# Optimization experiments

Hardware: AMD Instinct MI355X
Metric: run time of the kernel (lower is better)

## Reference

```python
import jax, jax.numpy as jnp
import numpy as np

HEAD = 16
H_DIM = 64  # dims // head
ROT = 32    # h_dim // 2


def setup_inputs() -> dict:
    key = jax.random.key(0)
    k1, k2, k3, k4 = jax.random.split(key, 4)
    B, S, D = 8, 4096, 1024
    x = jax.random.normal(k1, (B, S, D), dtype=jnp.float32)
    thetas = jax.random.normal(k2, (ROT,), dtype=jnp.float32) * 0.1
    theta_scale = jnp.ones((1,), dtype=jnp.float32)
    # near-orthogonal matrix, as r_matrix is initialized to eye
    r_matrix = jnp.eye(H_DIM, dtype=jnp.float32) + 0.01 * jax.random.normal(k3, (H_DIM, H_DIM), dtype=jnp.float32)
    base = 10000.0
    inv_freq = (1.0 / base ** (jnp.arange(0, H_DIM, 2, dtype=jnp.float32) / H_DIM)).astype(jnp.float32)
    # rotation plane index pairs (i, j) with i != j, as produced by update_pairs()
    i_idx = jax.random.randint(k4, (ROT,), 0, H_DIM)
    off = jax.random.randint(jax.random.fold_in(k4, 1), (ROT,), 1, H_DIM)
    j_idx = (i_idx + off) % H_DIM
    pairs = jnp.stack([i_idx, j_idx], axis=1).astype(jnp.int32)
    return {"x": x, "thetas": thetas, "theta_scale": theta_scale,
            "r_matrix": r_matrix, "inv_freq": inv_freq, "pairs": pairs}


def _blended_rotation(xf, pairs, thetas_scaled):
    """Apply rot sequential blended Givens rotations to xf [N, H_DIM].

    B = (G + H + R)/3 with G == R the Givens rotation in plane (i,j) and
    H = I - 2 v v^T (v = [cos, sin] in plane (i,j), ||v|| = 1).
    x @ B only changes columns i and j; all other columns pass through
    since (2*x_k + x_k)/3 = x_k. This is mathematically identical to the
    original dense h_dim x h_dim matmul per step.
    """
    def step(xc, inp):
        i, j, th = inp["i"], inp["j"], inp["th"]
        c, s = jnp.cos(th), jnp.sin(th)
        xi = jnp.take(xc, i, axis=1)
        xj = jnp.take(xc, j, axis=1)
        gi = xi * c + xj * s        # (x @ G) column i; also equals x . v
        gj = -xi * s + xj * c       # (x @ G) column j
        ni = (2.0 * gi + xi - 2.0 * gi * c) / 3.0
        nj = (2.0 * gj + xj - 2.0 * gi * s) / 3.0
        xc = xc.at[:, i].set(ni)
        xc = xc.at[:, j].set(nj)
        return xc, None
    xf, _ = jax.lax.scan(step, xf, {"i": pairs[:, 0], "j": pairs[:, 1], "th": thetas_scaled})
    return xf


def reference(x, thetas, theta_scale, r_matrix, inv_freq, pairs):
    B, S, D = x.shape
    xf = x.reshape(-1, H_DIM)                       # [B*S*head, h_dim]
    # adjusted_rot = int(round(rot_scale * rot)) == rot for rot_scale = 1
    xf = _blended_rotation(xf, pairs, thetas * theta_scale[0])
    xf = xf @ r_matrix
    xr = xf.reshape(B, S, HEAD, H_DIM)
    # RoPE-style sin/cos mix (note: concatenated halves, not interleaved)
    pos = jnp.arange(S, dtype=x.dtype)
    sinu = pos[:, None] * inv_freq[None, :]          # [S, h_dim/2]
    sin = jnp.sin(sinu)[None, :, None, :]
    cos = jnp.cos(sinu)[None, :, None, :]
    x1, x2 = xr[..., ::2], xr[..., 1::2]
    out = jnp.concatenate([x1 * cos - x2 * sin, x1 * sin + x2 * cos], axis=-1)
    return out.reshape(B, S, D)
```

## Files before the change

kernel.cpp:

```cpp
#include <hip/hip_runtime.h>

#define HEADS 16
#define HD 64
#define ROT 32
#define SEQ 4096
#define BROWS 256
#define PADW 33

typedef float sv16 __attribute__((ext_vector_type(16)));

__global__ __launch_bounds__(256) void build_W_kernel(
    const float* __restrict__ thetas,
    const float* __restrict__ theta_scale,
    const float* __restrict__ r_matrix,
    const int* __restrict__ pairs,
    float* __restrict__ Wp)
{
    __shared__ float M[64][65];
    __shared__ float Rl[64][65];
    const int tid = threadIdx.x;

    #pragma unroll
    for (int it = 0; it < 16; ++it) {
        const int f = it * 256 + tid;
        Rl[f >> 6][f & 63] = r_matrix[f];
    }

    if (tid < 64) {
        const int t = tid;
        #pragma unroll
        for (int k = 0; k < 64; ++k) M[t][k] = (k == t) ? 1.0f : 0.0f;
        const float scale = theta_scale[0];
        #pragma unroll 1
        for (int r = 0; r < ROT; ++r) {
            const int i = pairs[2 * r + 0];
            const int j = pairs[2 * r + 1];
            const float th = thetas[r] * scale;
            float s, c;
            sincosf(th, &s, &c);
            const float xi = M[t][i];
            const float xj = M[t][j];
            const float gi =  xi * c + xj * s;
            const float gj = -xi * s + xj * c;
            const float ni = (2.0f * gi + xi - 2.0f * gi * c) / 3.0f;
            const float nj = (2.0f * gj + xj - 2.0f * gi * s) / 3.0f;
            M[t][i] = ni;
            M[t][j] = nj;
        }
    }
    __syncthreads();

    const int n = tid & 63;
    const int kq = tid >> 6;
    const int cn = (n < 32) ? (2 * n) : (2 * (n - 32) + 1);
    #pragma unroll 1
    for (int kk = 0; kk < 16; ++kk) {
        const int k = kq * 16 + kk;
        float acc = 0.0f;
        #pragma unroll
        for (int j = 0; j < 64; ++j) acc = fmaf(M[k][j], Rl[j][cn], acc);
        Wp[k * 64 + n] = acc;
    }
}

__global__ __launch_bounds__(256, 4) void fused_main(
    const float* __restrict__ x,
    const float* __restrict__ Wp,
    const float* __restrict__ inv_freq,
    float* __restrict__ out)
{
    __shared__ float xs[BROWS * PADW];
    __shared__ float tc[16 * 33];
    __shared__ float tsn[16 * 33];

    const int tid = threadIdx.x;
    const int blk = blockIdx.x;
    const long long base4 = (long long)blk * (BROWS * HD / 4);
    const float4* __restrict__ xv = (const float4*)x + base4;
    float4* __restrict__ ov = (float4*)out + base4;

    {
        const int s0 = (blk & (SEQ / 16 - 1)) * 16;
        #pragma unroll
        for (int u = 0; u < 2; ++u) {
            const int e = tid * 2 + u;
            const int sl = e >> 5;
            const int f = e & 31;
            const float ang = (float)(s0 + sl) * inv_freq[f];
            float sn, cs;
            sincosf(ang, &sn, &cs);
            tc[sl * 33 + f] = cs;
            tsn[sl * 33 + f] = sn;
        }
    }

    float acc[64];
    #pragma unroll
    for (int nn = 0; nn < 64; ++nn) acc[nn] = 0.0f;

    #pragma unroll 1
    for (int half = 0; half < 2; ++half) {
        __syncthreads();
        #pragma unroll
        for (int it = 0; it < 8; ++it) {
            const int f = it * 256 + tid;
            const int row = f >> 3;
            const int c4 = f & 7;
            const float4 v = xv[row * 16 + half * 8 + c4];
            float* p = &xs[row * PADW + c4 * 4];
            p[0] = v.x; p[1] = v.y; p[2] = v.z; p[3] = v.w;
        }
        __syncthreads();

        const float* xrow = &xs[tid * PADW];
        #pragma unroll 1
        for (int kc = 0; kc < 2; ++kc) {
            float xk[16];
            #pragma unroll
            for (int m = 0; m < 16; ++m) xk[m] = xrow[kc * 16 + m];
            const int kbase = half * 32 + kc * 16;
            #pragma unroll
            for (int m = 0; m < 16; ++m) {
                const float* pm = Wp + (kbase + m) * 64;
                sv16 w0, w1, w2, w3;
                asm volatile(
                    "s_load_dwordx16 %0, %4, 0x0\n\t"
                    "s_load_dwordx16 %1, %4, 0x40\n\t"
                    "s_load_dwordx16 %2, %4, 0x80\n\t"
                    "s_load_dwordx16 %3, %4, 0xC0\n\t"
                    "s_waitcnt lgkmcnt(0)"
                    : "=&s"(w0), "=&s"(w1), "=&s"(w2), "=&s"(w3)
                    : "s"(pm));
                const float xm = xk[m];
                #pragma unroll
                for (int i = 0; i < 16; ++i) {
                    acc[i]      = fmaf(xm, w0[i], acc[i]);
                    acc[16 + i] = fmaf(xm, w1[i], acc[16 + i]);
                    acc[32 + i] = fmaf(xm, w2[i], acc[32 + i]);
                    acc[48 + i] = fmaf(xm, w3[i], acc[48 + i]);
                }
            }
        }
    }

    {
        const int sl = tid >> 4;
        #pragma unroll
        for (int n = 0; n < 32; ++n) {
            const float c = tc[sl * 33 + n];
            const float s = tsn[sl * 33 + n];
            const float a = acc[n];
            const float b = acc[32 + n];
            acc[n]      = a * c - b * s;
            acc[32 + n] = a * s + b * c;
        }
    }

    #pragma unroll 1
    for (int half = 0; half < 2; ++half) {
        __syncthreads();
        float* prow = &xs[tid * PADW];
        #pragma unroll
        for (int n = 0; n < 32; ++n) prow[n] = acc[half * 32 + n];
        __syncthreads();
        #pragma unroll
        for (int it = 0; it < 8; ++it) {
            const int f = it * 256 + tid;
            const int row = f >> 3;
            const int c4 = f & 7;
            const float* p = &xs[row * PADW + c4 * 4];
            ov[row * 16 + half * 8 + c4] = make_float4(p[0], p[1], p[2], p[3]);
        }
    }
}

extern "C" void kernel_launch(void* const* d_in, const int* in_sizes, int n_in,
                              void* d_out, int out_size, void* d_ws, size_t ws_size,
                              hipStream_t stream) {
    const float* x   = (const float*)d_in[0];
    const float* th  = (const float*)d_in[1];
    const float* sc  = (const float*)d_in[2];
    const float* R   = (const float*)d_in[3];
    const float* ivf = (const float*)d_in[4];
    const int*   pr  = (const int*)d_in[5];
    float* W = (float*)d_ws;

    build_W_kernel<<<1, 256, 0, stream>>>(th, sc, R, pr, W);

    const int rows = out_size / HD;
    const int blocks = rows / BROWS;
    fused_main<<<blocks, 256, 0, stream>>>(x, W, ivf, (float*)d_out);
}
```

Measured before the change: 342.6 us.

## Double-buffer scalar W loads and drop LDS staging for direct row I/O

The main kernel now double-buffers the scalar W row loads, so the next pair of rows is fetched while FMAs run on the current pair. Previously every row waited on all four loads before computing. It also removes the shared-memory staging of x and out: each thread reads and writes its own 64-float row directly as float4, and occupancy is raised to 5 blocks per CU. The W-builder kernel precomputes sincos and pair indices into shared memory in parallel. The risk is uncoalesced per-thread strided global access (256-byte row stride across lanes) and higher register pressure.

```diff
diff --git a/kernel.cpp b/kernel.cpp
--- a/kernel.cpp
+++ b/kernel.cpp
@@ -5,7 +5,6 @@
 #define ROT 32
 #define SEQ 4096
 #define BROWS 256
-#define PADW 33
 
 typedef float sv16 __attribute__((ext_vector_type(16)));
 
@@ -18,26 +17,36 @@
 {
     __shared__ float M[64][65];
     __shared__ float Rl[64][65];
+    __shared__ int   ip[32], jp[32];
+    __shared__ float cs[32], sn[32];
     const int tid = threadIdx.x;
 
+    if (tid < 32) {
+        const int i = pairs[2 * tid + 0];
+        const int j = pairs[2 * tid + 1];
+        float s, c;
+        sincosf(thetas[tid] * theta_scale[0], &s, &c);
+        ip[tid] = i; jp[tid] = j; cs[tid] = c; sn[tid] = s;
+    }
     #pragma unroll
     for (int it = 0; it < 16; ++it) {
         const int f = it * 256 + tid;
         Rl[f >> 6][f & 63] = r_matrix[f];
     }
+    if (tid < 64) {
+        #pragma unroll
+        for (int k = 0; k < 64; ++k) M[tid][k] = (k == tid) ? 1.0f : 0.0f;
+    }
+    __syncthreads();
 
     if (tid < 64) {
         const int t = tid;
-        #pragma unroll
-        for (int k = 0; k < 64; ++k) M[t][k] = (k == t) ? 1.0f : 0.0f;
-        const float scale = theta_scale[0];
         #pragma unroll 1
         for (int r = 0; r < ROT; ++r) {
-            const int i = pairs[2 * r + 0];
-            const int j = pairs[2 * r + 1];
-            const float th = thetas[r] * scale;
-            float s, c;
-            sincosf(th, &s, &c);
+            const int i = ip[r];
+            const int j = jp[r];
+            const float c = cs[r];
+            const float s = sn[r];
             const float xi = M[t][i];
             const float xj = M[t][j];
             const float gi =  xi * c + xj * s;
@@ -63,21 +72,34 @@
     }
 }
 
-__global__ __launch_bounds__(256, 4) void fused_main(
+#define PREF(C0, C1, OA, OB) asm volatile(                       \
+    "s_load_dwordx16 %0, %2, " #OA "\n\t"                         \
+    "s_load_dwordx16 %1, %2, " #OB                                \
+    : "=&s"(C0), "=&s"(C1) : "s"(wq))
+
+#define WAITW(C0, C1) asm volatile("s_waitcnt lgkmcnt(0)" : "+s"(C0), "+s"(C1))
+
+#define FMA32(C0, C1, M, H) do { const float xm_ = xkf[M];        \
+    _Pragma("unroll")                                             \
+    for (int i_ = 0; i_ < 16; ++i_) {                             \
+        acc[(H)*32 + i_]      = fmaf(xm_, (C0)[i_], acc[(H)*32 + i_]);      \
+        acc[(H)*32 + 16 + i_] = fmaf(xm_, (C1)[i_], acc[(H)*32 + 16 + i_]); \
+    } } while (0)
+
+__global__ __launch_bounds__(256, 5) void fused_main(
     const float* __restrict__ x,
     const float* __restrict__ Wp,
     const float* __restrict__ inv_freq,
     float* __restrict__ out)
 {
-    __shared__ float xs[BROWS * PADW];
     __shared__ float tc[16 * 33];
     __shared__ float tsn[16 * 33];
 
     const int tid = threadIdx.x;
     const int blk = blockIdx.x;
-    const long long base4 = (long long)blk * (BROWS * HD / 4);
-    const float4* __restrict__ xv = (const float4*)x + base4;
-    float4* __restrict__ ov = (float4*)out + base4;
+    const long long row = (long long)blk * BROWS + tid;
+    const float4* __restrict__ xp4 = (const float4*)(x + row * HD);
+    float4* __restrict__ op4 = (float4*)(out + row * HD);
 
     {
         const int s0 = (blk & (SEQ / 16 - 1)) * 16;
@@ -87,60 +109,67 @@
             const int sl = e >> 5;
             const int f = e & 31;
             const float ang = (float)(s0 + sl) * inv_freq[f];
-            float sn, cs;
-            sincosf(ang, &sn, &cs);
-            tc[sl * 33 + f] = cs;
-            tsn[sl * 33 + f] = sn;
-        }
-    }
+            float s_, c_;
+            sincosf(ang, &s_, &c_);
+            tc[sl * 33 + f] = c_;
+            tsn[sl * 33 + f] = s_;
+        }
+    }
+    __syncthreads();
 
     float acc[64];
     #pragma unroll
     for (int nn = 0; nn < 64; ++nn) acc[nn] = 0.0f;
 
     #pragma unroll 1
-    for (int half = 0; half < 2; ++half) {
-        __syncthreads();
-        #pragma unroll
-        for (int it = 0; it < 8; ++it) {
-            const int f = it * 256 + tid;
-            const int row = f >> 3;
-            const int c4 = f & 7;
-            const float4 v = xv[row * 16 + half * 8 + c4];
-            float* p = &xs[row * PADW + c4 * 4];
-            p[0] = v.x; p[1] = v.y; p[2] = v.z; p[3] = v.w;
-        }
-        __syncthreads();
-
-        const float* xrow = &xs[tid * PADW];
-        #pragma unroll 1
-        for (int kc = 0; kc < 2; ++kc) {
-            float xk[16];
-            #pragma unroll
-            for (int m = 0; m < 16; ++m) xk[m] = xrow[kc * 16 + m];
-            const int kbase = half * 32 + kc * 16;
-            #pragma unroll
-            for (int m = 0; m < 16; ++m) {
-                const float* pm = Wp + (kbase + m) * 64;
-                sv16 w0, w1, w2, w3;
-                asm volatile(
-                    "s_load_dwordx16 %0, %4, 0x0\n\t"
-                    "s_load_dwordx16 %1, %4, 0x40\n\t"
-                    "s_load_dwordx16 %2, %4, 0x80\n\t"
-                    "s_load_dwordx16 %3, %4, 0xC0\n\t"
-                    "s_waitcnt lgkmcnt(0)"
-                    : "=&s"(w0), "=&s"(w1), "=&s"(w2), "=&s"(w3)
-                    : "s"(pm));
-                const float xm = xk[m];
-                #pragma unroll
-                for (int i = 0; i < 16; ++i) {
-                    acc[i]      = fmaf(xm, w0[i], acc[i]);
-                    acc[16 + i] = fmaf(xm, w1[i], acc[16 + i]);
-                    acc[32 + i] = fmaf(xm, w2[i], acc[32 + i]);
-                    acc[48 + i] = fmaf(xm, w3[i], acc[48 + i]);
-                }
-            }
-        }
+    for (int q = 0; q < 4; ++q) {
+        float xkf[16];
+        {
+            const float4 t0 = xp4[q * 4 + 0];
+            const float4 t1 = xp4[q * 4 + 1];
+            const float4 t2 = xp4[q * 4 + 2];
+            const float4 t3 = xp4[q * 4 + 3];
+            xkf[0]=t0.x;  xkf[1]=t0.y;  xkf[2]=t0.z;  xkf[3]=t0.w;
+            xkf[4]=t1.x;  xkf[5]=t1.y;  xkf[6]=t1.z;  xkf[7]=t1.w;
+            xkf[8]=t2.x;  xkf[9]=t2.y;  xkf[10]=t2.z; xkf[11]=t2.w;
+            xkf[12]=t3.x; xkf[13]=t3.y; xkf[14]=t3.z; xkf[15]=t3.w;
+        }
+        const float* wq = Wp + q * 1024;
+        sv16 A0, A1, B0, B1;
+
+        PREF(A0, A1, 0, 64);            WAITW(A0, A1);
+        PREF(B0, B1, 128, 192);   FMA32(A0, A1, 0, 0);  WAITW(B0, B1);
+        PREF(A0, A1, 256, 320);   FMA32(B0, B1, 0, 1);  WAITW(A0, A1);
+        PREF(B0, B1, 384, 448);   FMA32(A0, A1, 1, 0);  WAITW(B0, B1);
+        PREF(A0, A1, 512, 576);   FMA32(B0, B1, 1, 1);  WAITW(A0, A1);
+        PREF(B0, B1, 640, 704);   FMA32(A0, A1, 2, 0);  WAITW(B0, B1);
+        PREF(A0, A1, 768, 832);   FMA32(B0, B1, 2, 1);  WAITW(A0, A1);
+        PREF(B0, B1, 896, 960);   FMA32(A0, A1, 3, 0);  WAITW(B0, B1);
+        PREF(A0, A1, 1024, 1088); FMA32(B0, B1, 3, 1);  WAITW(A0, A1);
+        PREF(B0, B1, 1152, 1216); FMA32(A0, A1, 4, 0);  WAITW(B0, B1);
+        PREF(A0, A1, 1280, 1344); FMA32(B0, B1, 4, 1);  WAITW(A0, A1);
+        PREF(B0, B1, 1408, 1472); FMA32(A0, A1, 5, 0);  WAITW(B0, B1);
+        PREF(A0, A1, 1536, 1600); FMA32(B0, B1, 5, 1);  WAITW(A0, A1);
+        PREF(B0, B1, 1664, 1728); FMA32(A0, A1, 6, 0);  WAITW(B0, B1);
+        PREF(A0, A1, 1792, 1856); FMA32(B0, B1, 6, 1);  WAITW(A0, A1);
+        PREF(B0, B1, 1920, 1984); FMA32(A0, A1, 7, 0);  WAITW(B0, B1);
+        PREF(A0, A1, 2048, 2112); FMA32(B0, B1, 7, 1);  WAITW(A0, A1);
+        PREF(B0, B1, 2176, 2240); FMA32(A0, A1, 8, 0);  WAITW(B0, B1);
+        PREF(A0, A1, 2304, 2368); FMA32(B0, B1, 8, 1);  WAITW(A0, A1);
+        PREF(B0, B1, 2432, 2496); FMA32(A0, A1, 9, 0);  WAITW(B0, B1);
+        PREF(A0, A1, 2560, 2624); FMA32(B0, B1, 9, 1);  WAITW(A0, A1);
+        PREF(B0, B1, 2688, 2752); FMA32(A0, A1, 10, 0); WAITW(B0, B1);
+        PREF(A0, A1, 2816, 2880); FMA32(B0, B1, 10, 1); WAITW(A0, A1);
+        PREF(B0, B1, 2944, 3008); FMA32(A0, A1, 11, 0); WAITW(B0, B1);
+        PREF(A0, A1, 3072, 3136); FMA32(B0, B1, 11, 1); WAITW(A0, A1);
+        PREF(B0, B1, 3200, 3264); FMA32(A0, A1, 12, 0); WAITW(B0, B1);
+        PREF(A0, A1, 3328, 3392); FMA32(B0, B1, 12, 1); WAITW(A0, A1);
+        PREF(B0, B1, 3456, 3520); FMA32(A0, A1, 13, 0); WAITW(B0, B1);
+        PREF(A0, A1, 3584, 3648); FMA32(B0, B1, 13, 1); WAITW(A0, A1);
+        PREF(B0, B1, 3712, 3776); FMA32(A0, A1, 14, 0); WAITW(B0, B1);
+        PREF(A0, A1, 3840, 3904); FMA32(B0, B1, 14, 1); WAITW(A0, A1);
+        PREF(B0, B1, 3968, 4032); FMA32(A0, A1, 15, 0); WAITW(B0, B1);
+        FMA32(B0, B1, 15, 1);
     }
 
     {
@@ -156,21 +185,10 @@
         }
     }
 
-    #pragma unroll 1
-    for (int half = 0; half < 2; ++half) {
-        __syncthreads();
-        float* prow = &xs[tid * PADW];
-        #pragma unroll
-        for (int n = 0; n < 32; ++n) prow[n] = acc[half * 32 + n];
-        __syncthreads();
-        #pragma unroll
-        for (int it = 0; it < 8; ++it) {
-            const int f = it * 256 + tid;
-            const int row = f >> 3;
-            const int c4 = f & 7;
-            const float* p = &xs[row * PADW + c4 * 4];
-            ov[row * 16 + half * 8 + c4] = make_float4(p[0], p[1], p[2], p[3]);
-        }
+    #pragma unroll
+    for (int c = 0; c < 16; ++c) {
+        op4[c] = make_float4(acc[4 * c + 0], acc[4 * c + 1],
+                             acc[4 * c + 2], acc[4 * c + 3]);
     }
 }
 
```

Measured after the change: 347.0 us. Within noise of the previous version (+1.3%).
